# Kernel optimization log

Measured on AMD Instinct MI355X. Metric: run time of the kernel, lower is better.

Reference implementation:

```python
import jax, jax.numpy as jnp
import numpy as np

K = 64                      # sort-pool k
B_GRAPHS, N_PER = 256, 512  # graphs, nodes per graph
DIM_F, E_PER = 128, 8192    # node feature dim, edges per graph
EMB = 32


def setup_inputs() -> dict:
    key = jax.random.key(0)
    ks = jax.random.split(key, 12)
    N = B_GRAPHS * N_PER
    off = (jnp.arange(B_GRAPHS) * N_PER)[:, None]
    x = jax.random.normal(ks[0], (N, DIM_F), jnp.float32)
    edge_src = (jax.random.randint(ks[1], (B_GRAPHS, E_PER), 0, N_PER) + off).reshape(-1)
    edge_dst = (jax.random.randint(ks[2], (B_GRAPHS, E_PER), 0, N_PER) + off).reshape(-1)

    def lin(k, o, i):
        return (jax.random.normal(k, (o, i), jnp.float32) / np.float32(np.sqrt(i)))

    return {
        "x": x,
        "W0": lin(ks[3], EMB, DIM_F), "b0": jnp.zeros((EMB,), jnp.float32),
        "W1": lin(ks[4], EMB, EMB),   "b1": jnp.zeros((EMB,), jnp.float32),
        "W2": lin(ks[5], EMB, EMB),   "b2": jnp.zeros((EMB,), jnp.float32),
        "W3": lin(ks[6], 1, EMB),     "b3": jnp.zeros((1,), jnp.float32),
        "conv1_w": jax.random.normal(ks[7], (16, 1, 97), jnp.float32) / np.float32(np.sqrt(97.0)),
        "conv1_b": jnp.zeros((16,), jnp.float32),
        "conv2_w": jax.random.normal(ks[8], (32, 16, 5), jnp.float32) / np.float32(np.sqrt(80.0)),
        "conv2_b": jnp.zeros((32,), jnp.float32),
        "d1_w": lin(ks[9], 128, 896),  "d1_b": jnp.zeros((128,), jnp.float32),
        "d2_w": lin(ks[10], 10, 128),  "d2_b": jnp.zeros((10,), jnp.float32),
        "edge_src": edge_src, "edge_dst": edge_dst,
        "num_graphs": B_GRAPHS,
    }


def _dgcnn_conv(h_in, W, b, src, dst):
    # h = lin(x); message = (1/deg_src)[dst] * h[src]; scatter-add at dst
    N = h_in.shape[0]
    h = h_in @ W.T + b
    deg = jax.ops.segment_sum(jnp.ones_like(src, dtype=h.dtype), src, num_segments=N)
    norm = 1.0 / deg                       # self-loops guarantee deg >= 1
    msg = h[src] * norm[dst][:, None]      # [E+N, C]
    return jax.ops.segment_sum(msg, dst, num_segments=N)


def _forward(x, W0, b0, W1, b1, W2, b2, W3, b3,
             conv1_w, conv1_b, conv2_w, conv2_b,
             d1_w, d1_b, d2_w, d2_b, src, dst, num_graphs):
    N = x.shape[0]
    self_idx = jnp.arange(N)
    src = jnp.concatenate([src, self_idx])   # add_self_loops
    dst = jnp.concatenate([dst, self_idx])
    hs = []
    h = x
    for (W, b) in ((W0, b0), (W1, b1), (W2, b2), (W3, b3)):
        h = jnp.tanh(_dgcnn_conv(h, W, b, src, dst))
        hs.append(h)
    feat = jnp.concatenate(hs, axis=1)       # [N, 97]
    D = feat.shape[1]
    B = num_graphs
    n = N // B
    g = feat.reshape(B, n, D)
    # global_sort_pool: sort nodes per graph by last channel, descending, take top-k
    order = jnp.argsort(-g[:, :, -1], axis=1)[:, :K]
    topk = jnp.take_along_axis(g, order[:, :, None], axis=1)   # [B, K, D]
    # Conv1d(1,16,kernel=D,stride=D) over [B,1,K*D] == per-node linear on D
    c1 = jax.nn.relu(jnp.einsum('bkd,od->bok', topk, conv1_w[:, 0, :])
                     + conv1_b[None, :, None])                  # [B,16,K]
    p = c1.reshape(B, 16, K // 2, 2).max(axis=-1)               # MaxPool1d(2,2)
    c2 = jax.lax.conv_general_dilated(p, conv2_w, (1,), 'VALID',
                                      dimension_numbers=('NCH', 'OIH', 'NCH'))
    c2 = jax.nn.relu(c2 + conv2_b[None, :, None])               # [B,32,28]
    flat = c2.reshape(B, -1)                                    # [B,896]
    hid = jax.nn.relu(flat @ d1_w.T + d1_b)                     # dropout = identity (eval)
    return hid @ d2_w.T + d2_b                                  # [B,10]


def reference(x, W0, b0, W1, b1, W2, b2, W3, b3,
              conv1_w, conv1_b, conv2_w, conv2_b,
              d1_w, d1_b, d2_w, d2_b, edge_src, edge_dst, num_graphs):
    return _forward(x, W0, b0, W1, b1, W2, b2, W3, b3,
                    conv1_w, conv1_b, conv2_w, conv2_b,
                    d1_w, d1_b, d2_w, d2_b, edge_src, edge_dst, num_graphs)
```

## Files before the change

kernel.cpp:

```cpp
#include <hip/hip_runtime.h>

#define NG   256
#define NP   512
#define EPG  8192
#define FDIM 128
#define STB  36

#define OFF_STAGE 0
#define OFF_BUFB  65536
#define OFF_CSR   139264
#define OFF_OFFS  155648
#define OFF_WT    156680
#define OFF_CUR   156712
#define OFF_PAD   158760
#define OFF_DCNT  158768
#define OFF_NRM   160816
#define SMEM_SZ   162864

#define OFF_L3    OFF_CUR
#define OFF_KEY   OFF_DCNT
#define OFF_RANKP OFF_CSR
#define OFF_TIDX  (OFF_CSR + 2048)
#define OFF_TKEY  (OFF_CSR + 2304)
#define FO_FEAT 0
#define FO_P    6208
#define FO_C2   6720
#define FO_HID  7616

__global__ __launch_bounds__(1024, 4) void dgcnn_fused(
    const float* __restrict__ x,
    const float* __restrict__ W0, const float* __restrict__ b0,
    const float* __restrict__ W1, const float* __restrict__ b1,
    const float* __restrict__ W2, const float* __restrict__ b2,
    const float* __restrict__ W3, const float* __restrict__ b3,
    const float* __restrict__ c1w, const float* __restrict__ c1b,
    const float* __restrict__ c2w, const float* __restrict__ c2b,
    const float* __restrict__ d1w, const float* __restrict__ d1b,
    const float* __restrict__ d2w, const float* __restrict__ d2b,
    const int* __restrict__ esrc, const int* __restrict__ edst,
    float* __restrict__ hs2,
    float* __restrict__ out)
{
  extern __shared__ char smem[];
  float*          stageF = (float*)(smem + OFF_STAGE);
  float*          bufB  = (float*)(smem + OFF_BUFB);
  unsigned short* csr   = (unsigned short*)(smem + OFF_CSR);
  unsigned short* offs  = (unsigned short*)(smem + OFF_OFFS);
  unsigned int*   wt    = (unsigned int*)(smem + OFF_WT);
  unsigned int*   cur   = (unsigned int*)(smem + OFF_CUR);
  unsigned int*   dcnt  = (unsigned int*)(smem + OFF_DCNT);
  float*          nrm   = (float*)(smem + OFF_NRM);
  float*          lin3S = (float*)(smem + OFF_L3);
  float*          keyA  = (float*)(smem + OFF_KEY);
  unsigned short* rankP = (unsigned short*)(smem + OFF_RANKP);
  unsigned short* topIdx= (unsigned short*)(smem + OFF_TIDX);
  float*          topKey= (float*)(smem + OFF_TKEY);

  const int g    = blockIdx.x;
  const int tid  = threadIdx.x;
  const int lane = tid & 63;
  const int wv   = __builtin_amdgcn_readfirstlane(tid >> 6);
  const int half = __builtin_amdgcn_readfirstlane(tid >> 9);
  const int v    = tid & 511;
  const int nb   = g * NP;

  const int ldRow0 = tid >> 3;
  const int ldGrp  = tid & 7;
  const int ldSwz  = (ldGrp ^ (ldRow0 & 7)) * 16;
  auto load_chunk = [&](int kc, float4* xr) {
    const float* base = x + (size_t)nb * FDIM + kc * 32 + ldGrp * 4;
#pragma unroll
    for (int it = 0; it < 4; it++)
      xr[it] = *(const float4*)(base + (size_t)(ldRow0 + it * 128) * FDIM);
  };
  auto store_chunk = [&](const float4* xr) {
#pragma unroll
    for (int it = 0; it < 4; it++)
      *(float4*)(smem + OFF_STAGE + (ldRow0 + it * 128) * 128 + ldSwz) = xr[it];
  };

  float4 xr[4], xr2[4];
  load_chunk(0, xr);
  const int eb = g * EPG;
  const int4* s4p = (const int4*)(esrc + eb);
  const int4* d4p = (const int4*)(edst + eb);
  const int4 sa = s4p[tid], sb = s4p[tid + 1024];
  const int4 da = d4p[tid], db = d4p[tid + 1024];

  int es[8], ed[8];
  es[0]=sa.x-nb; es[1]=sa.y-nb; es[2]=sa.z-nb; es[3]=sa.w-nb;
  es[4]=sb.x-nb; es[5]=sb.y-nb; es[6]=sb.z-nb; es[7]=sb.w-nb;
  ed[0]=da.x-nb; ed[1]=da.y-nb; ed[2]=da.z-nb; ed[3]=da.w-nb;
  ed[4]=db.x-nb; ed[5]=db.y-nb; ed[6]=db.z-nb; ed[7]=db.w-nb;

  if (tid < 512) { cur[tid] = 0u; dcnt[tid] = 0u; }

  float acc0[16];
#pragma unroll
  for (int c = 0; c < 16; c++) acc0[c] = b0[half * 16 + c];
  const char* rowp = smem + OFF_STAGE + v * 128;
  const int vswz = v & 7;

  auto compute_chunk = [&](const int kc) {
#pragma unroll
    for (int jg = 0; jg < 8; jg++) {
      const float4 t = *(const float4*)(rowp + ((jg ^ vswz) * 16));
#pragma unroll
      for (int c = 0; c < 16; c++) {
        const float* wr = W0 + (size_t)(half * 16 + c) * FDIM + kc * 32 + jg * 4;
        acc0[c] = fmaf(t.x, wr[0], acc0[c]);
        acc0[c] = fmaf(t.y, wr[1], acc0[c]);
        acc0[c] = fmaf(t.z, wr[2], acc0[c]);
        acc0[c] = fmaf(t.w, wr[3], acc0[c]);
      }
    }
  };

  __syncthreads();
  store_chunk(xr);
  load_chunk(1, xr2);
  __syncthreads();
#pragma unroll
  for (int i = 0; i < 8; i++) {
    atomicAdd(&dcnt[es[i]], 1u);
    atomicAdd(&dcnt[ed[i]], 65536u);
  }
  compute_chunk(0);
#pragma unroll
  for (int it = 0; it < 4; it++) xr[it] = xr2[it];
  __syncthreads();
  store_chunk(xr);
  load_chunk(2, xr2);
  __syncthreads();
  unsigned c_scan = 0;
  if (tid < 512) {
    const unsigned cw = dcnt[tid];
    nrm[tid] = 1.0f / (float)((cw & 0xFFFFu) + 1u);
    c_scan = cw >> 16;
    for (int d = 1; d < 64; d <<= 1) {
      const unsigned t = __shfl_up(c_scan, (unsigned)d, 64);
      if (lane >= d) c_scan += t;
    }
    if (lane == 63) wt[wv] = c_scan;
  }
  compute_chunk(1);
#pragma unroll
  for (int it = 0; it < 4; it++) xr[it] = xr2[it];
  __syncthreads();
  store_chunk(xr);
  load_chunk(3, xr2);
  __syncthreads();
  if (tid < 512) {
    unsigned base = 0;
    for (int w = 0; w < wv; w++) base += wt[w];
    offs[tid + 1] = (unsigned short)(base + c_scan);
    if (tid == 0) offs[0] = 0;
  }
  compute_chunk(2);
  __syncthreads();
  store_chunk(xr2);
  __syncthreads();
#pragma unroll
  for (int i = 0; i < 8; i++) {
    const unsigned pos = (unsigned)offs[ed[i]] + atomicAdd(&cur[ed[i]], 1u);
    csr[pos] = (unsigned short)es[i];
  }
  compute_chunk(3);
  {
    float4* br = (float4*)(bufB + v * STB + half * 16);
#pragma unroll
    for (int j = 0; j < 4; j++)
      br[j] = make_float4(acc0[j*4+0], acc0[j*4+1], acc0[j*4+2], acc0[j*4+3]);
  }
  __syncthreads();

  float h[16];
  auto do_agg = [&]() {
    float4 A0, A1, A2, A3;
    const float4* sr = (const float4*)(bufB + v * STB + half * 16);
    A0 = sr[0]; A1 = sr[1]; A2 = sr[2]; A3 = sr[3];
    const int e0 = offs[v], e1 = offs[v + 1];
    int e = e0;
    for (; e + 3 < e1; e += 4) {
      const int s0 = csr[e], s1 = csr[e + 1], s2 = csr[e + 2], s3 = csr[e + 3];
      const float4* rb0 = (const float4*)(bufB + s0 * STB + half * 16);
      const float4* rb1 = (const float4*)(bufB + s1 * STB + half * 16);
      const float4* rb2 = (const float4*)(bufB + s2 * STB + half * 16);
      const float4* rb3 = (const float4*)(bufB + s3 * STB + half * 16);
      const float4 p0 = rb0[0], p1 = rb0[1], p2 = rb0[2], p3 = rb0[3];
      const float4 q0 = rb1[0], q1 = rb1[1], q2 = rb1[2], q3 = rb1[3];
      const float4 r0 = rb2[0], r1 = rb2[1], r2 = rb2[2], r3 = rb2[3];
      const float4 t0 = rb3[0], t1 = rb3[1], t2 = rb3[2], t3 = rb3[3];
      A0.x += p0.x + q0.x; A0.y += p0.y + q0.y; A0.z += p0.z + q0.z; A0.w += p0.w + q0.w;
      A1.x += p1.x + q1.x; A1.y += p1.y + q1.y; A1.z += p1.z + q1.z; A1.w += p1.w + q1.w;
      A2.x += p2.x + q2.x; A2.y += p2.y + q2.y; A2.z += p2.z + q2.z; A2.w += p2.w + q2.w;
      A3.x += p3.x + q3.x; A3.y += p3.y + q3.y; A3.z += p3.z + q3.z; A3.w += p3.w + q3.w;
      A0.x += r0.x + t0.x; A0.y += r0.y + t0.y; A0.z += r0.z + t0.z; A0.w += r0.w + t0.w;
      A1.x += r1.x + t1.x; A1.y += r1.y + t1.y; A1.z += r1.z + t1.z; A1.w += r1.w + t1.w;
      A2.x += r2.x + t2.x; A2.y += r2.y + t2.y; A2.z += r2.z + t2.z; A2.w += r2.w + t2.w;
      A3.x += r3.x + t3.x; A3.y += r3.y + t3.y; A3.z += r3.z + t3.z; A3.w += r3.w + t3.w;
    }
    for (; e + 1 < e1; e += 2) {
      const int s0 = csr[e], s1 = csr[e + 1];
      const float4* rb0 = (const float4*)(bufB + s0 * STB + half * 16);
      const float4* rb1 = (const float4*)(bufB + s1 * STB + half * 16);
      const float4 p0 = rb0[0], p1 = rb0[1], p2 = rb0[2], p3 = rb0[3];
      const float4 q0 = rb1[0], q1 = rb1[1], q2 = rb1[2], q3 = rb1[3];
      A0.x += p0.x + q0.x; A0.y += p0.y + q0.y; A0.z += p0.z + q0.z; A0.w += p0.w + q0.w;
      A1.x += p1.x + q1.x; A1.y += p1.y + q1.y; A1.z += p1.z + q1.z; A1.w += p1.w + q1.w;
      A2.x += p2.x + q2.x; A2.y += p2.y + q2.y; A2.z += p2.z + q2.z; A2.w += p2.w + q2.w;
      A3.x += p3.x + q3.x; A3.y += p3.y + q3.y; A3.z += p3.z + q3.z; A3.w += p3.w + q3.w;
    }
    if (e < e1) {
      const int s = csr[e];
      const float4* rb = (const float4*)(bufB + s * STB + half * 16);
      const float4 r0 = rb[0], r1 = rb[1], r2 = rb[2], r3 = rb[3];
      A0.x += r0.x; A0.y += r0.y; A0.z += r0.z; A0.w += r0.w;
      A1.x += r1.x; A1.y += r1.y; A1.z += r1.z; A1.w += r1.w;
      A2.x += r2.x; A2.y += r2.y; A2.z += r2.z; A2.w += r2.w;
      A3.x += r3.x; A3.y += r3.y; A3.z += r3.z; A3.w += r3.w;
    }
    const float nv = nrm[v];
    h[0]=tanhf(A0.x*nv); h[1]=tanhf(A0.y*nv); h[2]=tanhf(A0.z*nv); h[3]=tanhf(A0.w*nv);
    h[4]=tanhf(A1.x*nv); h[5]=tanhf(A1.y*nv); h[6]=tanhf(A1.z*nv); h[7]=tanhf(A1.w*nv);
    h[8]=tanhf(A2.x*nv); h[9]=tanhf(A2.y*nv); h[10]=tanhf(A2.z*nv); h[11]=tanhf(A2.w*nv);
    h[12]=tanhf(A3.x*nv); h[13]=tanhf(A3.y*nv); h[14]=tanhf(A3.z*nv); h[15]=tanhf(A3.w*nv);
  };

  auto put_h = [&]() {
    float4* br = (float4*)(bufB + v * STB + half * 16);
#pragma unroll
    for (int j = 0; j < 4; j++)
      br[j] = make_float4(h[j*4+0], h[j*4+1], h[j*4+2], h[j*4+3]);
  };

  auto store_h1 = [&]() {
#pragma unroll
    for (int c = 0; c < 16; c++)
      stageF[(half * 16 + c) * 512 + v] = h[c];
  };

  auto spill2 = [&]() {
    float4* dst = (float4*)(hs2 + (size_t)(nb + v) * 32 + half * 16);
#pragma unroll
    for (int j = 0; j < 4; j++)
      dst[j] = make_float4(h[j*4+0], h[j*4+1], h[j*4+2], h[j*4+3]);
  };

  auto lin_core = [&](const float* hf, const float* __restrict__ W, const float* __restrict__ b) {
    float acc[16];
#pragma unroll
    for (int c = 0; c < 16; c++) {
      const int C = half * 16 + c;
      const float* wr = W + C * 32;
      float a = b[C];
#pragma unroll
      for (int j = 0; j < 32; j++) a = fmaf(hf[j], wr[j], a);
      acc[c] = a;
    }
    float4* br = (float4*)(bufB + v * STB + half * 16);
#pragma unroll
    for (int j = 0; j < 4; j++)
      br[j] = make_float4(acc[j*4+0], acc[j*4+1], acc[j*4+2], acc[j*4+3]);
  };

  do_agg();
  store_h1();
  __syncthreads();
  {
    float hf[32];
#pragma unroll
    for (int j = 0; j < 32; j++) hf[j] = stageF[j * 512 + v];
    lin_core(hf, W1, b1);
  }
  __syncthreads();
  do_agg();
  spill2();
  __syncthreads();
  {
    float hf[32];
    const float4* rr = (const float4*)(hs2 + (size_t)(nb + v) * 32);
#pragma unroll
    for (int j = 0; j < 8; j++) {
      const float4 t = rr[j];
      hf[4*j]=t.x; hf[4*j+1]=t.y; hf[4*j+2]=t.z; hf[4*j+3]=t.w;
    }
    lin_core(hf, W2, b2);
  }
  __syncthreads();
  do_agg();
  __syncthreads();
  put_h();
  __syncthreads();

  if (tid < 512) {
    const float4* rr = (const float4*)(bufB + tid * STB);
    double a = (double)b3[0];
#pragma unroll
    for (int j = 0; j < 8; j++) {
      const float4 t = rr[j];
      a = fma((double)t.x, (double)W3[j*4+0], a);
      a = fma((double)t.y, (double)W3[j*4+1], a);
      a = fma((double)t.z, (double)W3[j*4+2], a);
      a = fma((double)t.w, (double)W3[j*4+3], a);
    }
    lin3S[tid] = (float)a;
  }
  __syncthreads();
  if (tid < 512) {
    double a = (double)lin3S[tid];
    const int e0 = offs[tid], e1 = offs[tid + 1];
    for (int e = e0; e < e1; e++) a += (double)lin3S[csr[e]];
    a *= (double)nrm[tid];
    keyA[tid] = tanhf((float)a);
  }
  __syncthreads();

  {
    const int i = tid & 511;
    const int p = tid >> 9;
    const float ki = keyA[i];
    const float4* k4 = (const float4*)(keyA + p * 256);
    int cnt = 0;
#pragma unroll 8
    for (int jj = 0; jj < 64; jj++) {
      const float4 kv = k4[jj];
      const int j0 = p * 256 + jj * 4;
      cnt += (kv.x > ki || (kv.x == ki && (j0    ) < i)) ? 1 : 0;
      cnt += (kv.y > ki || (kv.y == ki && (j0 + 1) < i)) ? 1 : 0;
      cnt += (kv.z > ki || (kv.z == ki && (j0 + 2) < i)) ? 1 : 0;
      cnt += (kv.w > ki || (kv.w == ki && (j0 + 3) < i)) ? 1 : 0;
    }
    rankP[tid] = (unsigned short)cnt;
  }
  __syncthreads();
  if (tid < 512) {
    const int r = (int)rankP[tid] + (int)rankP[tid + 512];
    if (r < 64) { topIdx[r] = (unsigned short)tid; topKey[r] = keyA[tid]; }
  }
  __syncthreads();

  {
    const int k = lane;
    const int t = wv;
    const int node = (int)topIdx[k];
    const float a0 = stageF[ t       * 512 + node];
    const float a1 = stageF[(t + 16) * 512 + node];
    const float* h2row = hs2 + (size_t)(nb + node) * 32;
    const float b0v = h2row[t];
    const float b1v = h2row[t + 16];
    const float* brow = bufB + node * STB;
    const float c0v = brow[t];
    const float c1v = brow[t + 16];
    const float kk = topKey[k];
    __syncthreads();
    float* featS = bufB + FO_FEAT;
    featS[ t        * 64 + k] = a0;
    featS[(t + 16)  * 64 + k] = a1;
    featS[(t + 32)  * 64 + k] = b0v;
    featS[(t + 48)  * 64 + k] = b1v;
    featS[(t + 64)  * 64 + k] = c0v;
    featS[(t + 80)  * 64 + k] = c1v;
    if (t == 0) featS[96 * 64 + k] = kk;
  }
  __syncthreads();

  {
    const float* featS = bufB + FO_FEAT;
    float* ps = bufB + FO_P;
    const int ch = wv;
    float a = c1b[ch];
    const float* wr = c1w + ch * 97;
    for (int d = 0; d < 97; d++)
      a = fmaf(featS[d * 64 + lane], wr[d], a);
    a = fmaxf(a, 0.f);
    const float m  = fmaxf(a, __shfl_down(a, 1, 64));
    const float pv = __shfl(m, (lane & 31) * 2, 64);
    if (lane < 32) ps[ch * 32 + lane] = pv;
  }
  __syncthreads();

  {
    const float* ps  = bufB + FO_P;
    float* c2s = bufB + FO_C2;
    const int o = wv;
    if (lane < 28) {
      float a0 = 0.f, a1 = 0.f;
      for (int i = 0; i < 16; i++) {
#pragma unroll
        for (int r = 0; r < 5; r++) {
          const float pv = ps[i * 32 + lane + r];
          a0 = fmaf(pv, c2w[((o     ) * 16 + i) * 5 + r], a0);
          a1 = fmaf(pv, c2w[((o + 16) * 16 + i) * 5 + r], a1);
        }
      }
      c2s[(o     ) * 28 + lane] = fmaxf(a0 + c2b[o     ], 0.f);
      c2s[(o + 16) * 28 + lane] = fmaxf(a1 + c2b[o + 16], 0.f);
    }
  }
  __syncthreads();

  {
    const float* c2s  = bufB + FO_C2;
    float* hids = bufB + FO_HID;
    float fl[14];
#pragma unroll
    for (int j = 0; j < 14; j++) fl[j] = c2s[lane + j * 64];
#pragma unroll 2
    for (int hh = 0; hh < 8; hh++) {
      const int hI = wv * 8 + hh;
      const float* wr = d1w + (size_t)hI * 896;
      float a = 0.f;
#pragma unroll
      for (int j = 0; j < 14; j++) a = fmaf(fl[j], wr[lane + j * 64], a);
#pragma unroll
      for (int m = 32; m > 0; m >>= 1) a += __shfl_xor(a, m, 64);
      if (lane == 0) hids[hI] = fmaxf(a + d1b[hI], 0.f);
    }
  }
  __syncthreads();

  if (tid < 10) {
    const float* hids = bufB + FO_HID;
    const float* wr = d2w + tid * 128;
    double a = (double)d2b[tid];
#pragma unroll 8
    for (int hh = 0; hh < 128; hh++) a = fma((double)hids[hh], (double)wr[hh], a);
    out[g * 10 + tid] = (float)a;
  }
}

extern "C" void kernel_launch(void* const* d_in, const int* in_sizes, int n_in,
                              void* d_out, int out_size, void* d_ws, size_t ws_size,
                              hipStream_t stream) {
  const float* x   = (const float*)d_in[0];
  const float* W0  = (const float*)d_in[1];
  const float* b0  = (const float*)d_in[2];
  const float* W1  = (const float*)d_in[3];
  const float* b1  = (const float*)d_in[4];
  const float* W2  = (const float*)d_in[5];
  const float* b2  = (const float*)d_in[6];
  const float* W3  = (const float*)d_in[7];
  const float* b3  = (const float*)d_in[8];
  const float* c1w = (const float*)d_in[9];
  const float* c1b = (const float*)d_in[10];
  const float* c2w = (const float*)d_in[11];
  const float* c2b = (const float*)d_in[12];
  const float* d1w = (const float*)d_in[13];
  const float* d1b = (const float*)d_in[14];
  const float* d2w = (const float*)d_in[15];
  const float* d2b = (const float*)d_in[16];
  const int* esrc  = (const int*)d_in[17];
  const int* edst  = (const int*)d_in[18];

  float* hs2 = (float*)d_ws;
  float* outp = (float*)d_out;

  hipFuncSetAttribute(reinterpret_cast<const void*>(dgcnn_fused),
                      hipFuncAttributeMaxDynamicSharedMemorySize, SMEM_SZ);
  dgcnn_fused<<<NG, 1024, SMEM_SZ, stream>>>(x, W0, b0, W1, b1, W2, b2, W3, b3,
                                             c1w, c1b, c2w, c2b, d1w, d1b, d2w, d2b,
                                             esrc, edst, hs2, outp);
}
```

Baseline: 276.5 us.

## Sort nodes by in-degree to balance aggregation work across wavefront lanes

```diff
diff --git a/kernel.cpp b/kernel.cpp
--- a/kernel.cpp
+++ b/kernel.cpp
@@ -15,10 +15,12 @@
 #define OFF_PAD   158760
 #define OFF_DCNT  158768
 #define OFF_NRM   160816
-#define SMEM_SZ   162864
+#define OFF_BINS  162864
+#define SMEM_SZ   163248
 
 #define OFF_L3    OFF_CUR
-#define OFF_KEY   OFF_DCNT
+#define OFF_PERM  OFF_DCNT
+#define OFF_KEY   OFF_NRM
 #define OFF_RANKP OFF_CSR
 #define OFF_TIDX  (OFF_CSR + 2048)
 #define OFF_TKEY  (OFF_CSR + 2304)
@@ -50,6 +52,8 @@
   unsigned int*   cur   = (unsigned int*)(smem + OFF_CUR);
   unsigned int*   dcnt  = (unsigned int*)(smem + OFF_DCNT);
   float*          nrm   = (float*)(smem + OFF_NRM);
+  unsigned int*   bins  = (unsigned int*)(smem + OFF_BINS);
+  unsigned short* perm  = (unsigned short*)(smem + OFF_PERM);
   float*          lin3S = (float*)(smem + OFF_L3);
   float*          keyA  = (float*)(smem + OFF_KEY);
   unsigned short* rankP = (unsigned short*)(smem + OFF_RANKP);
@@ -94,12 +98,14 @@
   ed[4]=db.x-nb; ed[5]=db.y-nb; ed[6]=db.z-nb; ed[7]=db.w-nb;
 
   if (tid < 512) { cur[tid] = 0u; dcnt[tid] = 0u; }
+  if (tid < 96)  bins[tid] = 0u;
 
   float acc0[16];
 #pragma unroll
   for (int c = 0; c < 16; c++) acc0[c] = b0[half * 16 + c];
   const char* rowp = smem + OFF_STAGE + v * 128;
   const int vswz = v & 7;
+  int mydeg = 0;
 
   auto compute_chunk = [&](const int kc) {
 #pragma unroll
@@ -137,6 +143,7 @@
     const unsigned cw = dcnt[tid];
     nrm[tid] = 1.0f / (float)((cw & 0xFFFFu) + 1u);
     c_scan = cw >> 16;
+    mydeg = (int)(cw >> 16);
     for (int d = 1; d < 64; d <<= 1) {
       const unsigned t = __shfl_up(c_scan, (unsigned)d, 64);
       if (lane >= d) c_scan += t;
@@ -155,6 +162,8 @@
     for (int w = 0; w < wv; w++) base += wt[w];
     offs[tid + 1] = (unsigned short)(base + c_scan);
     if (tid == 0) offs[0] = 0;
+    const int dd = mydeg > 47 ? 47 : mydeg;
+    atomicAdd(&bins[dd], 1u);
   }
   compute_chunk(2);
   __syncthreads();
@@ -165,6 +174,15 @@
     const unsigned pos = (unsigned)offs[ed[i]] + atomicAdd(&cur[ed[i]], 1u);
     csr[pos] = (unsigned short)es[i];
   }
+  if (wv == 15) {
+    const unsigned bc = (lane < 48) ? bins[lane] : 0u;
+    unsigned sc = bc;
+    for (int d = 1; d < 64; d <<= 1) {
+      const unsigned t2 = __shfl_up(sc, (unsigned)d, 64);
+      if (lane >= d) sc += t2;
+    }
+    if (lane < 48) bins[48 + lane] = sc - bc;
+  }
   compute_chunk(3);
   {
     float4* br = (float4*)(bufB + v * STB + half * 16);
@@ -173,13 +191,21 @@
       br[j] = make_float4(acc0[j*4+0], acc0[j*4+1], acc0[j*4+2], acc0[j*4+3]);
   }
   __syncthreads();
+
+  if (tid < 512) {
+    const int dd = mydeg > 47 ? 47 : mydeg;
+    const unsigned c = atomicSub(&bins[dd], 1u);
+    perm[bins[48 + dd] + c - 1u] = (unsigned short)tid;
+  }
+  __syncthreads();
+  const int u = (int)perm[v];
 
   float h[16];
   auto do_agg = [&]() {
     float4 A0, A1, A2, A3;
-    const float4* sr = (const float4*)(bufB + v * STB + half * 16);
+    const float4* sr = (const float4*)(bufB + u * STB + half * 16);
     A0 = sr[0]; A1 = sr[1]; A2 = sr[2]; A3 = sr[3];
-    const int e0 = offs[v], e1 = offs[v + 1];
+    const int e0 = offs[u], e1 = offs[u + 1];
     int e = e0;
     for (; e + 3 < e1; e += 4) {
       const int s0 = csr[e], s1 = csr[e + 1], s2 = csr[e + 2], s3 = csr[e + 3];
@@ -220,7 +246,7 @@
       A2.x += r2.x; A2.y += r2.y; A2.z += r2.z; A2.w += r2.w;
       A3.x += r3.x; A3.y += r3.y; A3.z += r3.z; A3.w += r3.w;
     }
-    const float nv = nrm[v];
+    const float nv = nrm[u];
     h[0]=tanhf(A0.x*nv); h[1]=tanhf(A0.y*nv); h[2]=tanhf(A0.z*nv); h[3]=tanhf(A0.w*nv);
     h[4]=tanhf(A1.x*nv); h[5]=tanhf(A1.y*nv); h[6]=tanhf(A1.z*nv); h[7]=tanhf(A1.w*nv);
     h[8]=tanhf(A2.x*nv); h[9]=tanhf(A2.y*nv); h[10]=tanhf(A2.z*nv); h[11]=tanhf(A2.w*nv);
@@ -228,7 +254,7 @@
   };
 
   auto put_h = [&]() {
-    float4* br = (float4*)(bufB + v * STB + half * 16);
+    float4* br = (float4*)(bufB + u * STB + half * 16);
 #pragma unroll
     for (int j = 0; j < 4; j++)
       br[j] = make_float4(h[j*4+0], h[j*4+1], h[j*4+2], h[j*4+3]);
@@ -237,11 +263,11 @@
   auto store_h1 = [&]() {
 #pragma unroll
     for (int c = 0; c < 16; c++)
-      stageF[(half * 16 + c) * 512 + v] = h[c];
+      stageF[(half * 16 + c) * 512 + u] = h[c];
   };
 
   auto spill2 = [&]() {
-    float4* dst = (float4*)(hs2 + (size_t)(nb + v) * 32 + half * 16);
+    float4* dst = (float4*)(hs2 + (size_t)(nb + u) * 32 + half * 16);
 #pragma unroll
     for (int j = 0; j < 4; j++)
       dst[j] = make_float4(h[j*4+0], h[j*4+1], h[j*4+2], h[j*4+3]);
@@ -308,11 +334,11 @@
   }
   __syncthreads();
   if (tid < 512) {
-    double a = (double)lin3S[tid];
-    const int e0 = offs[tid], e1 = offs[tid + 1];
+    double a = (double)lin3S[u];
+    const int e0 = offs[u], e1 = offs[u + 1];
     for (int e = e0; e < e1; e++) a += (double)lin3S[csr[e]];
-    a *= (double)nrm[tid];
-    keyA[tid] = tanhf((float)a);
+    a *= (double)nrm[u];
+    keyA[u] = tanhf((float)a);
   }
   __syncthreads();
 
```

Result: no change. 274.8 us (-0.6%).
